# Kernel tuning notes

Hardware: AMD Instinct MI355X
Metric: run time of the kernel (lower is better)

The kernel has to match this reference:

```python
import jax, jax.numpy as jnp
import numpy as np

E4M3_AMAX = 216.0   # HPU constant: 240 * 0.9
FP8_MAX = 240.0     # saturation bound used by cast_to_fp8 on HPU e4m3


def _quant_fp8(x, scale):
    """Dynamic per-tensor fp8 quantize: scale, saturate, round-to-fp8, back to f32."""
    y = jnp.clip(x * scale, -FP8_MAX, FP8_MAX)
    return y.astype(jnp.float8_e4m3fn).astype(jnp.float32)


def setup_inputs() -> dict:
    key = jax.random.key(0)
    k1, k2, k3 = jax.random.split(key, 3)
    inp = jax.random.normal(k1, (4, 4096, 4096), dtype=jnp.float32)
    weight = jax.random.normal(k2, (4096, 4096), dtype=jnp.float32) * 0.02
    bias = jax.random.normal(k3, (4096,), dtype=jnp.float32)
    return {"inp": inp, "weight": weight, "bias": bias}


def reference(inp, weight, bias):
    # weight quantization (done once at init in the torch module; same math)
    w_scale = E4M3_AMAX / jnp.max(jnp.abs(weight))
    w8 = _quant_fp8(weight, w_scale)                      # [out, in]
    # dynamic activation quantization (per forward call)
    i_scale = E4M3_AMAX / jnp.max(jnp.abs(inp))
    x2d = inp.reshape(-1, weight.shape[1])                # [tokens, in]
    x8 = _quant_fp8(x2d, i_scale)
    # fp8_gemm_v2: dequantize by the inverse scales in the epilogue, add bias
    out = (x8 @ w8.T) * (1.0 / i_scale) * (1.0 / w_scale) + bias  # [tokens, out]
    return out.reshape(*inp.shape[:-1], out.shape[-1])
```

## Files before the change

kernel.cpp:

```cpp
#include <hip/hip_runtime.h>

typedef unsigned char u8;
typedef unsigned int u32;
using f32x4 = __attribute__((ext_vector_type(4))) float;

#define E4M3_AMAX 216.0f
#define FP8_MAXV 240.0f

#define BM 128
#define BN 128
#define BK 64

#define GLD_LDS16(g, l) \
    __builtin_amdgcn_global_load_lds((const __attribute__((address_space(1))) void*)(g), \
                                     (__attribute__((address_space(3))) void*)(l), 16, 0, 0)

__global__ void maxabs2_kernel(const float* __restrict__ a, long na4, u32* __restrict__ outa,
                               const float* __restrict__ b, long nb4, u32* __restrict__ outb,
                               int blocksA) {
    const float4* x4;
    long n4;
    u32* out;
    long bid, nb;
    if ((int)blockIdx.x < blocksA) {
        x4 = (const float4*)a; n4 = na4; out = outa; bid = blockIdx.x; nb = blocksA;
    } else {
        x4 = (const float4*)b; n4 = nb4; out = outb; bid = blockIdx.x - blocksA; nb = gridDim.x - blocksA;
    }
    long stride = nb * blockDim.x;
    long i = bid * blockDim.x + threadIdx.x;
    u32 m = 0;
    for (long j = i; j < n4; j += stride) {
        float4 v = x4[j];
        u32 pa = __float_as_uint(fabsf(v.x));
        u32 pb = __float_as_uint(fabsf(v.y));
        u32 pc = __float_as_uint(fabsf(v.z));
        u32 pd = __float_as_uint(fabsf(v.w));
        m = pa > m ? pa : m;
        m = pb > m ? pb : m;
        m = pc > m ? pc : m;
        m = pd > m ? pd : m;
    }
    #pragma unroll
    for (int off = 32; off > 0; off >>= 1) {
        u32 o = (u32)__shfl_down((unsigned int)m, (unsigned int)off, 64);
        m = o > m ? o : m;
    }
    __shared__ u32 sm[8];
    int wave = threadIdx.x >> 6, lane = threadIdx.x & 63;
    if (lane == 0) sm[wave] = m;
    __syncthreads();
    if (threadIdx.x == 0) {
        u32 r = sm[0];
        int nw = blockDim.x >> 6;
        for (int w = 1; w < nw; ++w) r = sm[w] > r ? sm[w] : r;
        atomicMax(out, r);
    }
}

__global__ void quant2_kernel(const float* __restrict__ a, u8* __restrict__ ya, long na4,
                              const float* __restrict__ b, u8* __restrict__ yb, long nb4,
                              const u32* __restrict__ maxbits, int blocksA) {
    const float4* x4;
    int* y4;
    long n4, bid, nb;
    float mx;
    if ((int)blockIdx.x < blocksA) {
        x4 = (const float4*)a; y4 = (int*)ya; n4 = na4; bid = blockIdx.x; nb = blocksA;
        mx = __uint_as_float(maxbits[0]);
    } else {
        x4 = (const float4*)b; y4 = (int*)yb; n4 = nb4; bid = blockIdx.x - blocksA; nb = gridDim.x - blocksA;
        mx = __uint_as_float(maxbits[1]);
    }
    float scale = E4M3_AMAX / mx;
    long stride = nb * blockDim.x;
    long i = bid * blockDim.x + threadIdx.x;
    for (long j = i; j < n4; j += stride) {
        float4 v = x4[j];
        float pa = fminf(fmaxf(v.x * scale, -FP8_MAXV), FP8_MAXV);
        float pb = fminf(fmaxf(v.y * scale, -FP8_MAXV), FP8_MAXV);
        float pc = fminf(fmaxf(v.z * scale, -FP8_MAXV), FP8_MAXV);
        float pd = fminf(fmaxf(v.w * scale, -FP8_MAXV), FP8_MAXV);
        int p = 0;
        p = __builtin_amdgcn_cvt_pk_fp8_f32(pa, pb, p, false);
        p = __builtin_amdgcn_cvt_pk_fp8_f32(pc, pd, p, true);
        y4[j] = p;
    }
}

__device__ __forceinline__ void stage_tile(const u8* gA, const u8* gB, u8* lA, u8* lB, int K) {
    GLD_LDS16(gA,                  lA);
    GLD_LDS16(gA + (size_t)64 * K, lA + 4096);
    GLD_LDS16(gB,                  lB);
    GLD_LDS16(gB + (size_t)64 * K, lB + 4096);
}

__device__ __forceinline__ void compute_tile(const u8* Asb, const u8* Bsb, f32x4 acc[4][4],
                                             int wm, int wn, int fr, int quad, int swzr) {
    #pragma unroll
    for (int ks = 0; ks < 2; ++ks) {
        const int colx = (ks * 32 + quad * 8) ^ (swzr << 4);
        long a[4], b[4];
        #pragma unroll
        for (int i = 0; i < 4; ++i) {
            a[i] = *(const long*)(Asb + (wm + i * 16 + fr) * BK + colx);
            b[i] = *(const long*)(Bsb + (wn + i * 16 + fr) * BK + colx);
        }
        #pragma unroll
        for (int i = 0; i < 4; ++i)
            #pragma unroll
            for (int j = 0; j < 4; ++j)
                acc[i][j] = __builtin_amdgcn_mfma_f32_16x16x32_fp8_fp8(a[i], b[j], acc[i][j], 0, 0, 0);
    }
}

__global__ __launch_bounds__(256) void gemm_fp8_kernel(
    const u8* __restrict__ A,
    const u8* __restrict__ B,
    const float* __restrict__ bias,
    const u32* __restrict__ scales,
    float* __restrict__ C, int M, int N, int K)
{
    __shared__ u8 smem[2][2 * BM * BK];

    const int tid = threadIdx.x;
    const int wave = tid >> 6;
    const int lane = tid & 63;
    const int fr = lane & 15;
    const int quad = lane >> 4;

    const int bm = blockIdx.y * BM;
    const int bn = blockIdx.x * BN;

    const int wm = (wave >> 1) * 64;
    const int wn = (wave & 1) * 64;

    f32x4 acc[4][4] = {};

    const int srow = 16 * wave + (lane >> 2);
    const int swzs = (lane >> 3) & 3;
    const int scol = ((lane & 3) ^ swzs) * 16;
    const u8* gA = A + (size_t)(bm + srow) * K + scol;
    const u8* gB = B + (size_t)(bn + srow) * K + scol;
    const int lofs = wave * 1024;

    u8* As0 = smem[0];            u8* Bs0 = smem[0] + BM * BK;
    u8* As1 = smem[1];            u8* Bs1 = smem[1] + BM * BK;

    const int swzr = (fr >> 1) & 3;

    stage_tile(gA, gB, As0 + lofs, Bs0 + lofs, K);

    for (int k0 = 0; k0 < K; k0 += 2 * BK) {
        __syncthreads();
        if (k0 + BK < K)
            stage_tile(gA + (k0 + BK), gB + (k0 + BK), As1 + lofs, Bs1 + lofs, K);
        compute_tile(As0, Bs0, acc, wm, wn, fr, quad, swzr);

        __syncthreads();
        if (k0 + 2 * BK < K)
            stage_tile(gA + (k0 + 2 * BK), gB + (k0 + 2 * BK), As0 + lofs, Bs0 + lofs, K);
        compute_tile(As1, Bs1, acc, wm, wn, fr, quad, swzr);
    }

    const float mi = __uint_as_float(scales[0]);
    const float mw = __uint_as_float(scales[1]);
    const float i_scale = E4M3_AMAX / mi;
    const float w_scale = E4M3_AMAX / mw;
    const float deq = (1.0f / i_scale) * (1.0f / w_scale);

    #pragma unroll
    for (int i = 0; i < 4; ++i) {
        const int row0 = bm + wm + i * 16 + quad * 4;
        #pragma unroll
        for (int j = 0; j < 4; ++j) {
            const int col = bn + wn + j * 16 + fr;
            const float bv = bias[col];
            #pragma unroll
            for (int rg = 0; rg < 4; ++rg) {
                C[(size_t)(row0 + rg) * N + col] = acc[i][j][rg] * deq + bv;
            }
        }
    }
}

extern "C" void kernel_launch(void* const* d_in, const int* in_sizes, int n_in,
                              void* d_out, int out_size, void* d_ws, size_t ws_size,
                              hipStream_t stream) {
    const float* inp    = (const float*)d_in[0];
    const float* weight = (const float*)d_in[1];
    const float* bias   = (const float*)d_in[2];
    float* out = (float*)d_out;

    const int N = in_sizes[2];
    const int K = in_sizes[1] / N;
    const long icount = in_sizes[0];
    const int M = (int)(icount / K);
    const long wcount = (long)N * K;

    u32* scales = (u32*)d_ws;
    u8* x8 = (u8*)d_ws + 256;
    u8* w8 = x8 + (size_t)M * K;

    hipMemsetAsync(d_ws, 0, 16, stream);

    maxabs2_kernel<<<2560, 256, 0, stream>>>(inp, icount / 4, scales + 0,
                                             weight, wcount / 4, scales + 1, 2048);
    quant2_kernel<<<2560, 256, 0, stream>>>(inp, x8, icount / 4,
                                            weight, w8, wcount / 4, scales, 2048);

    dim3 grid(N / BN, M / BM);
    gemm_fp8_kernel<<<grid, 256, 0, stream>>>(x8, w8, bias, scales, out, M, N, K);
}
```

Baseline: 879.3 us.

## Triple-buffer GEMM LDS staging with partial vmcnt waits and raised MFMA priority

Result: no change. 890.8 us (+1.3%).

```diff
diff --git a/kernel.cpp b/kernel.cpp
--- a/kernel.cpp
+++ b/kernel.cpp
@@ -29,32 +29,25 @@
     }
     long stride = nb * blockDim.x;
     long i = bid * blockDim.x + threadIdx.x;
-    u32 m = 0;
+    float m = 0.0f;
     for (long j = i; j < n4; j += stride) {
         float4 v = x4[j];
-        u32 pa = __float_as_uint(fabsf(v.x));
-        u32 pb = __float_as_uint(fabsf(v.y));
-        u32 pc = __float_as_uint(fabsf(v.z));
-        u32 pd = __float_as_uint(fabsf(v.w));
-        m = pa > m ? pa : m;
-        m = pb > m ? pb : m;
-        m = pc > m ? pc : m;
-        m = pd > m ? pd : m;
+        float m01 = fmaxf(fabsf(v.x), fabsf(v.y));
+        float m23 = fmaxf(fabsf(v.z), fabsf(v.w));
+        m = fmaxf(m, fmaxf(m01, m23));
     }
     #pragma unroll
-    for (int off = 32; off > 0; off >>= 1) {
-        u32 o = (u32)__shfl_down((unsigned int)m, (unsigned int)off, 64);
-        m = o > m ? o : m;
-    }
-    __shared__ u32 sm[8];
+    for (int off = 32; off > 0; off >>= 1)
+        m = fmaxf(m, __shfl_down(m, off, 64));
+    __shared__ float sm[8];
     int wave = threadIdx.x >> 6, lane = threadIdx.x & 63;
     if (lane == 0) sm[wave] = m;
     __syncthreads();
     if (threadIdx.x == 0) {
-        u32 r = sm[0];
+        float r = sm[0];
         int nw = blockDim.x >> 6;
-        for (int w = 1; w < nw; ++w) r = sm[w] > r ? sm[w] : r;
-        atomicMax(out, r);
+        for (int w = 1; w < nw; ++w) r = fmaxf(r, sm[w]);
+        atomicMax(out, __float_as_uint(r));
     }
 }
 
@@ -121,7 +114,7 @@
     const u32* __restrict__ scales,
     float* __restrict__ C, int M, int N, int K)
 {
-    __shared__ u8 smem[2][2 * BM * BK];
+    __shared__ u8 smem[3][2 * BM * BK];
 
     const int tid = threadIdx.x;
     const int wave = tid >> 6;
@@ -144,23 +137,32 @@
     const u8* gB = B + (size_t)(bn + srow) * K + scol;
     const int lofs = wave * 1024;
 
-    u8* As0 = smem[0];            u8* Bs0 = smem[0] + BM * BK;
-    u8* As1 = smem[1];            u8* Bs1 = smem[1] + BM * BK;
-
     const int swzr = (fr >> 1) & 3;
 
-    stage_tile(gA, gB, As0 + lofs, Bs0 + lofs, K);
-
-    for (int k0 = 0; k0 < K; k0 += 2 * BK) {
-        __syncthreads();
-        if (k0 + BK < K)
-            stage_tile(gA + (k0 + BK), gB + (k0 + BK), As1 + lofs, Bs1 + lofs, K);
-        compute_tile(As0, Bs0, acc, wm, wn, fr, quad, swzr);
-
-        __syncthreads();
-        if (k0 + 2 * BK < K)
-            stage_tile(gA + (k0 + 2 * BK), gB + (k0 + 2 * BK), As0 + lofs, Bs0 + lofs, K);
-        compute_tile(As1, Bs1, acc, wm, wn, fr, quad, swzr);
+    const int NT = K / BK;
+
+    stage_tile(gA,      gB,      smem[0] + lofs, smem[0] + BM * BK + lofs, K);
+    stage_tile(gA + BK, gB + BK, smem[1] + lofs, smem[1] + BM * BK + lofs, K);
+
+    const u8* cB_ = smem[0];
+    const u8* nB_ = smem[1];
+    const u8* pB_ = smem[2];
+
+    for (int t = 0; t < NT; ++t) {
+        if (t < NT - 1) { asm volatile("s_waitcnt vmcnt(4)" ::: "memory"); }
+        else            { asm volatile("s_waitcnt vmcnt(0)" ::: "memory"); }
+        __builtin_amdgcn_s_barrier();
+        __builtin_amdgcn_sched_barrier(0);
+
+        if (t + 2 < NT)
+            stage_tile(gA + (size_t)(t + 2) * BK, gB + (size_t)(t + 2) * BK,
+                       (u8*)pB_ + lofs, (u8*)pB_ + BM * BK + lofs, K);
+
+        __builtin_amdgcn_s_setprio(1);
+        compute_tile(cB_, cB_ + BM * BK, acc, wm, wn, fr, quad, swzr);
+        __builtin_amdgcn_s_setprio(0);
+
+        const u8* tmp = cB_; cB_ = nB_; nB_ = pB_; pB_ = tmp;
     }
 
     const float mi = __uint_as_float(scales[0]);
```
